# Optimization experiments

Measured on AMD Instinct MI355X. Metric: run time of the kernel, lower is better.

The kernel has to match this reference:

```python
import jax, jax.numpy as jnp
import numpy as np

GROUPS = 32
N_HEADS = 8
EPS = 1e-5


def setup_inputs() -> dict:
    key = jax.random.key(0)
    ks = jax.random.split(key, 4)
    B, C, H, W = 8, 512, 32, 32
    x = jax.random.normal(ks[0], (B, C, H, W), dtype=jnp.float32)
    norm_scale = jnp.ones((C,), jnp.float32)
    norm_bias = jnp.zeros((C,), jnp.float32)
    qkv_w = jax.random.normal(ks[1], (3 * C, C), jnp.float32) * (C ** -0.5)
    qkv_b = jnp.zeros((3 * C,), jnp.float32)
    proj_w = jax.random.normal(ks[2], (C, C), jnp.float32) * (C ** -0.5)
    proj_b = jnp.zeros((C,), jnp.float32)
    return {"x": x, "norm_scale": norm_scale, "norm_bias": norm_bias,
            "qkv_w": qkv_w, "qkv_b": qkv_b, "proj_w": proj_w, "proj_b": proj_b}


def reference(x, norm_scale, norm_bias, qkv_w, qkv_b, proj_w, proj_b):
    B, C, H, W = x.shape
    T = H * W
    xf = x.reshape(B, C, T)

    # GroupNorm32 (32 groups, computed in float32, affine)
    xg = xf.astype(jnp.float32).reshape(B, GROUPS, C // GROUPS, T)
    mean = xg.mean(axis=(2, 3), keepdims=True)
    var = xg.var(axis=(2, 3), keepdims=True)
    xn = ((xg - mean) * jax.lax.rsqrt(var + EPS)).reshape(B, C, T)
    xn = (xn * norm_scale[:, None] + norm_bias[:, None]).astype(x.dtype)

    # qkv: 1x1 conv1d == pointwise matmul -> [B, 3C, T]
    qkv = jnp.einsum('oc,bct->bot', qkv_w, xn) + qkv_b[:, None]

    # QKVAttentionLegacy: reshape to [B*H, 3*ch, T], split
    ch = C // N_HEADS
    qkv_h = qkv.reshape(B * N_HEADS, 3 * ch, T)
    q, k, v = qkv_h[:, :ch], qkv_h[:, ch:2 * ch], qkv_h[:, 2 * ch:]
    scale = ch ** -0.25
    weight = jnp.einsum('bct,bcs->bts', q * scale, k * scale)  # [B*H, T, T]
    weight = jax.nn.softmax(weight.astype(jnp.float32), axis=-1).astype(qkv.dtype)
    a = jnp.einsum('bts,bcs->bct', weight, v).reshape(B, C, T)

    # proj_out (1x1 conv) + residual
    h = jnp.einsum('oc,bct->bot', proj_w, a) + proj_b[:, None]
    return (xf + h).reshape(B, C, H, W)
```

## Files before the change

### kernel.cpp

```cpp
#include <hip/hip_runtime.h>
#include <hip/hip_bf16.h>
#include <stdint.h>

typedef unsigned short u16;
typedef unsigned int u32;
typedef __bf16 bf16x8 __attribute__((ext_vector_type(8)));
typedef float f32x4 __attribute__((ext_vector_type(4)));


static __device__ __forceinline__ u16 f2bf(float f) {
  union { __hip_bfloat16 h; u16 u; } c;
  c.h = __float2bfloat16(f);
  return c.u;
}

static __device__ __forceinline__ void gload_lds16(const void* g, void* l) {
  __builtin_amdgcn_global_load_lds(
      (__attribute__((address_space(1))) u32*)(uintptr_t)g,
      (__attribute__((address_space(3))) u32*)l, 16, 0, 0);
}

__global__ __launch_bounds__(256) void wcvt(const float* __restrict__ wq,
                                            const float* __restrict__ wp,
                                            u16* __restrict__ wqb,
                                            u16* __restrict__ wpb) {
  int idx = (blockIdx.x * 256 + threadIdx.x) * 4;
  const float* s;
  u16* d;
  if (idx < 786432) { s = wq + idx; d = wqb + idx; }
  else { int k = idx - 786432; s = wp + k; d = wpb + k; }
  float4 v = *(const float4*)s;
  uint2 o;
  o.x = (u32)f2bf(v.x) | ((u32)f2bf(v.y) << 16);
  o.y = (u32)f2bf(v.z) | ((u32)f2bf(v.w) << 16);
  *(uint2*)d = o;
}

__global__ __launch_bounds__(256) void gn_stats(const float* __restrict__ x,
                                                float* __restrict__ st) {
  int bg = blockIdx.x;
  const float* p = x + (size_t)bg * 16384;
  float s1 = 0.f, s2 = 0.f;
  for (int i = threadIdx.x * 4; i < 16384; i += 1024) {
    float4 v = *(const float4*)(p + i);
    s1 += v.x + v.y + v.z + v.w;
    s2 += v.x * v.x + v.y * v.y + v.z * v.z + v.w * v.w;
  }
#pragma unroll
  for (int off = 1; off < 64; off <<= 1) {
    s1 += __shfl_xor(s1, off);
    s2 += __shfl_xor(s2, off);
  }
  __shared__ float r1[4], r2[4];
  int w = threadIdx.x >> 6, l = threadIdx.x & 63;
  if (l == 0) { r1[w] = s1; r2[w] = s2; }
  __syncthreads();
  if (threadIdx.x == 0) {
    float t1 = r1[0] + r1[1] + r1[2] + r1[3];
    float t2 = r2[0] + r2[1] + r2[2] + r2[3];
    float mean = t1 * (1.f / 16384.f);
    float var = t2 * (1.f / 16384.f) - mean * mean;
    st[bg * 2] = mean;
    st[bg * 2 + 1] = rsqrtf(var + 1e-5f);
  }
}

__global__ __launch_bounds__(256) void gn_apply(const float* __restrict__ x,
                                                const float* __restrict__ st,
                                                const float* __restrict__ ns,
                                                const float* __restrict__ nbi,
                                                u16* __restrict__ xnt) {
  __shared__ u16 tile[32 * 520];
  int b = blockIdx.x >> 5;
  int t0 = (blockIdx.x & 31) << 5;
  int tid = threadIdx.x;
  int tl = tid & 31, cg = tid >> 5;
#pragma unroll 4
  for (int cc = 0; cc < 64; ++cc) {
    int c = cc * 8 + cg;
    float mean = st[(b * 32 + (c >> 4)) * 2];
    float rstd = st[(b * 32 + (c >> 4)) * 2 + 1];
    float v = x[(size_t)b * 524288 + (size_t)c * 1024 + t0 + tl];
    float vn = (v - mean) * rstd * ns[c] + nbi[c];
    tile[tl * 520 + c] = f2bf(vn);
  }
  __syncthreads();
#pragma unroll
  for (int i = 0; i < 8; ++i) {
    int chunk = i * 256 + tid;
    int tl2 = chunk >> 6;
    int c0 = (chunk & 63) * 8;
    uint4 d = *(const uint4*)(tile + tl2 * 520 + c0);
    *(uint4*)(xnt + (size_t)b * 524288 + (size_t)(t0 + tl2) * 512 + c0) = d;
  }
}

static __device__ __forceinline__ void gemm_core(const u16* Abase, const u16* Bbase,
                                                 f32x4 acc[4][4], u16* As, u16* Bs,
                                                 int w, int l, int wm, int wn) {
  const int r8 = l >> 3, ch = l & 7;
  const int fr = l & 15, fq = l >> 4;
#pragma unroll 1
  for (int kt = 0; kt < 8; ++kt) {
    __syncthreads();
#pragma unroll
    for (int i = 0; i < 4; ++i) {
      int gi = (w << 2) + i;
      int row = (gi << 3) + r8;
      int xoff = ((ch ^ (row & 7)) << 4);
      gload_lds16((const char*)Abase + (size_t)row * 1024 + (kt << 7) + xoff,
                  (char*)As + (gi << 10));
      gload_lds16((const char*)Bbase + (size_t)row * 1024 + (kt << 7) + xoff,
                  (char*)Bs + (gi << 10));
    }
    __syncthreads();
#pragma unroll
    for (int kf = 0; kf < 2; ++kf) {
      bf16x8 af[4], bfv[4];
#pragma unroll
      for (int i = 0; i < 4; ++i) {
        int rowA = wm * 64 + i * 16 + fr;
        af[i] = *(const bf16x8*)(As + rowA * 64 + ((((kf << 2) + fq) ^ (rowA & 7)) << 3));
        int rowB = wn * 64 + i * 16 + fr;
        bfv[i] = *(const bf16x8*)(Bs + rowB * 64 + ((((kf << 2) + fq) ^ (rowB & 7)) << 3));
      }
#pragma unroll
      for (int i = 0; i < 4; ++i)
#pragma unroll
        for (int j = 0; j < 4; ++j)
          acc[i][j] = __builtin_amdgcn_mfma_f32_16x16x32_bf16(af[i], bfv[j], acc[i][j], 0, 0, 0);
    }
  }
}

__global__ __launch_bounds__(256) void gemm_qkv(const u16* __restrict__ Wq,
                                                const u16* __restrict__ Xnt,
                                                const float* __restrict__ bq,
                                                u16* __restrict__ qT,
                                                u16* __restrict__ kT,
                                                u16* __restrict__ vv) {
  __shared__ u16 As[128 * 64];
  __shared__ u16 Bs[128 * 64];
  int bid0 = blockIdx.x;
  int bid = (bid0 & 7) * 96 + (bid0 >> 3);
  int mb = bid % 12, nb = (bid / 12) % 8, b = bid / 96;
  int tid = threadIdx.x, w = tid >> 6, l = tid & 63;
  int wm = w >> 1, wn = w & 1;
  f32x4 acc[4][4];
#pragma unroll
  for (int i = 0; i < 4; ++i)
#pragma unroll
    for (int j = 0; j < 4; ++j) acc[i][j] = (f32x4){0.f, 0.f, 0.f, 0.f};

  gemm_core(Wq + (size_t)mb * 65536, Xnt + (size_t)b * 524288 + (size_t)nb * 65536,
            acc, As, Bs, w, l, wm, wn);

  int fr = l & 15, fq = l >> 4;
#pragma unroll
  for (int i = 0; i < 4; ++i) {
    int o0 = mb * 128 + wm * 64 + i * 16 + fq * 4;
    int h = o0 / 192, j0 = o0 % 192;
    int seg = j0 >> 6, off = j0 & 63;
    float qksc = (seg == 0) ? 0.51011687f : 0.35355339f;
    float b0 = bq[o0], b1 = bq[o0 + 1], b2 = bq[o0 + 2], b3 = bq[o0 + 3];
    size_t hb = (size_t)(b * 8 + h) * 65536;
#pragma unroll
    for (int j = 0; j < 4; ++j) {
      int t = nb * 128 + wn * 64 + j * 16 + fr;
      f32x4 v = acc[i][j];
      if (seg < 2) {
        u16* dst = (seg == 0 ? qT : kT) + hb + (size_t)t * 64 + off;
        uint2 pk;
        pk.x = (u32)f2bf((v[0] + b0) * qksc) | ((u32)f2bf((v[1] + b1) * qksc) << 16);
        pk.y = (u32)f2bf((v[2] + b2) * qksc) | ((u32)f2bf((v[3] + b3) * qksc) << 16);
        *(uint2*)dst = pk;
      } else {
        u16* dst = vv + hb + (size_t)off * 1024 + t;
        dst[0] = f2bf(v[0] + b0);
        dst[1024] = f2bf(v[1] + b1);
        dst[2048] = f2bf(v[2] + b2);
        dst[3072] = f2bf(v[3] + b3);
      }
    }
  }
}

__global__ __launch_bounds__(256) void attn(const u16* __restrict__ qT,
                                            const u16* __restrict__ kT,
                                            const u16* __restrict__ vv,
                                            u16* __restrict__ aT) {
  __shared__ u16 Ks[64 * 64];
  __shared__ u16 Vs[80 * 64];
  __shared__ u16 Ps[4 * 16 * 72];
  int bid = blockIdx.x;
  int bh = (bid & 7) * 8 + (bid >> 7);
  int tq = (bid >> 3) & 15;
  int tid = threadIdx.x, w = tid >> 6, l = tid & 63;
  int fr = l & 15, fq = l >> 4;
  int r8 = l >> 3, ch = l & 7;
  size_t hb = (size_t)bh * 65536;

  {
    int row = 64 + (tid >> 4);
    int c4 = (tid & 15) * 4;
    u16 val = (row == 64) ? (u16)0x3F80 : (u16)0;
    u16* p = Vs + row * 64 + c4;
    p[0] = val; p[1] = val; p[2] = val; p[3] = val;
  }

  bf16x8 aq[2];
  {
    const u16* qp = qT + hb + (size_t)(tq * 64 + w * 16 + fr) * 64 + fq * 8;
    aq[0] = *(const bf16x8*)(qp);
    aq[1] = *(const bf16x8*)(qp + 32);
  }

  f32x4 acc_o[4];
  f32x4 acc_s = (f32x4){0.f, 0.f, 0.f, 0.f};
#pragma unroll
  for (int nb = 0; nb < 4; ++nb) acc_o[nb] = (f32x4){0.f, 0.f, 0.f, 0.f};

  u16* pw = Ps + w * (16 * 72);

  for (int st = 0; st < 16; ++st) {
    __syncthreads();
#pragma unroll
    for (int i = 0; i < 2; ++i) {
      int gi = (w << 1) + i;
      int row = (gi << 3) + r8;
      int xoff = ((ch ^ (row & 7)) << 4);
      gload_lds16((const char*)(kT + hb) + (size_t)(st * 64 + row) * 128 + xoff,
                  (char*)Ks + (gi << 10));
      gload_lds16((const char*)(vv + hb) + (size_t)row * 2048 + st * 128 + xoff,
                  (char*)Vs + (gi << 10));
    }
    __syncthreads();

    f32x4 sa[4];
#pragma unroll
    for (int nb = 0; nb < 4; ++nb) sa[nb] = (f32x4){0.f, 0.f, 0.f, 0.f};
    __builtin_amdgcn_s_setprio(1);
#pragma unroll
    for (int nb = 0; nb < 4; ++nb) {
      int krow = nb * 16 + fr;
#pragma unroll
      for (int kf = 0; kf < 2; ++kf) {
        bf16x8 bk = *(const bf16x8*)(Ks + krow * 64 + ((((kf << 2) + fq) ^ (krow & 7)) << 3));
        sa[nb] = __builtin_amdgcn_mfma_f32_16x16x32_bf16(aq[kf], bk, sa[nb], 0, 0, 0);
      }
    }
    __builtin_amdgcn_s_setprio(0);

#pragma unroll
    for (int nb = 0; nb < 4; ++nb)
#pragma unroll
      for (int r = 0; r < 4; ++r)
        pw[(fq * 4 + r) * 72 + nb * 16 + fr] = f2bf(exp2f(sa[nb][r]));

    bf16x8 ap[2];
#pragma unroll
    for (int kf = 0; kf < 2; ++kf)
      ap[kf] = *(const bf16x8*)(pw + fr * 72 + kf * 32 + fq * 8);

    __builtin_amdgcn_s_setprio(1);
#pragma unroll
    for (int nb = 0; nb < 4; ++nb) {
      int vrow = nb * 16 + fr;
#pragma unroll
      for (int kf = 0; kf < 2; ++kf) {
        bf16x8 bv = *(const bf16x8*)(Vs + vrow * 64 + ((((kf << 2) + fq) ^ (vrow & 7)) << 3));
        acc_o[nb] = __builtin_amdgcn_mfma_f32_16x16x32_bf16(ap[kf], bv, acc_o[nb], 0, 0, 0);
      }
    }
    {
      int vrow = 64 + fr;
#pragma unroll
      for (int kf = 0; kf < 2; ++kf) {
        bf16x8 bv = *(const bf16x8*)(Vs + vrow * 64 + ((((kf << 2) + fq) ^ (vrow & 7)) << 3));
        acc_s = __builtin_amdgcn_mfma_f32_16x16x32_bf16(ap[kf], bv, acc_s, 0, 0, 0);
      }
    }
    __builtin_amdgcn_s_setprio(0);
  }

  int b = bh >> 3, h = bh & 7;
  f32x4 invl;
#pragma unroll
  for (int r = 0; r < 4; ++r) invl[r] = 1.f / __shfl(acc_s[r], l & 48);
#pragma unroll
  for (int nb = 0; nb < 4; ++nb) {
    f32x4 ov = acc_o[nb] * invl;
#pragma unroll
    for (int r = 0; r < 4; ++r) {
      int t = tq * 64 + w * 16 + fq * 4 + r;
      aT[(size_t)b * 524288 + (size_t)t * 512 + h * 64 + nb * 16 + fr] = f2bf(ov[r]);
    }
  }
}

__global__ __launch_bounds__(256) void gemm_proj(const u16* __restrict__ Wp,
                                                 const u16* __restrict__ aT,
                                                 const float* __restrict__ bp,
                                                 const float* __restrict__ x,
                                                 float* __restrict__ out) {
  __shared__ u16 As[128 * 64];
  __shared__ u16 Bs[128 * 64];
  int bid0 = blockIdx.x;
  int bid = (bid0 & 7) * 32 + (bid0 >> 3);
  int mb = bid & 3, nb = (bid >> 2) & 7, b = bid >> 5;
  int tid = threadIdx.x, w = tid >> 6, l = tid & 63;
  int wm = w >> 1, wn = w & 1;
  f32x4 acc[4][4];
#pragma unroll
  for (int i = 0; i < 4; ++i)
#pragma unroll
    for (int j = 0; j < 4; ++j) acc[i][j] = (f32x4){0.f, 0.f, 0.f, 0.f};

  gemm_core(Wp + (size_t)mb * 65536, aT + (size_t)b * 524288 + (size_t)nb * 65536,
            acc, As, Bs, w, l, wm, wn);

  int fr = l & 15, fq = l >> 4;
#pragma unroll
  for (int i = 0; i < 4; ++i) {
    int o0 = mb * 128 + wm * 64 + i * 16 + fq * 4;
    float b0 = bp[o0], b1 = bp[o0 + 1], b2 = bp[o0 + 2], b3 = bp[o0 + 3];
#pragma unroll
    for (int j = 0; j < 4; ++j) {
      int t = nb * 128 + wn * 64 + j * 16 + fr;
      f32x4 v = acc[i][j];
      size_t base = (size_t)b * 524288 + (size_t)o0 * 1024 + t;
      out[base] = x[base] + v[0] + b0;
      out[base + 1024] = x[base + 1024] + v[1] + b1;
      out[base + 2048] = x[base + 2048] + v[2] + b2;
      out[base + 3072] = x[base + 3072] + v[3] + b3;
    }
  }
}

extern "C" void kernel_launch(void* const* d_in, const int* in_sizes, int n_in,
                              void* d_out, int out_size, void* d_ws, size_t ws_size,
                              hipStream_t stream) {
  const float* x = (const float*)d_in[0];
  const float* ns = (const float*)d_in[1];
  const float* nbi = (const float*)d_in[2];
  const float* wq = (const float*)d_in[3];
  const float* bq = (const float*)d_in[4];
  const float* wp = (const float*)d_in[5];
  const float* bp = (const float*)d_in[6];
  float* out = (float*)d_out;
  char* ws = (char*)d_ws;

  u16* wqb = (u16*)(ws);
  u16* wpb = (u16*)(ws + 1572864);
  float* st = (float*)(ws + 2097152);
  u16* xnt = (u16*)(ws + 2101248);
  u16* qT = (u16*)(ws + 2101248 + 8388608);
  u16* kT = (u16*)(ws + 2101248 + 2 * 8388608);
  u16* vv = (u16*)(ws + 2101248 + 3 * 8388608);
  u16* aT = xnt;

  hipLaunchKernelGGL(wcvt, dim3(1024), dim3(256), 0, stream, wq, wp, wqb, wpb);
  hipLaunchKernelGGL(gn_stats, dim3(256), dim3(256), 0, stream, x, st);
  hipLaunchKernelGGL(gn_apply, dim3(256), dim3(256), 0, stream, x, st, ns, nbi, xnt);
  hipLaunchKernelGGL(gemm_qkv, dim3(768), dim3(256), 0, stream, wqb, xnt, bq, qT, kT, vv);
  hipLaunchKernelGGL(attn, dim3(1024), dim3(256), 0, stream, qT, kT, vv, aT);
  hipLaunchKernelGGL(gemm_proj, dim3(256), dim3(256), 0, stream, wpb, aT, bp, x, out);
}
```

Measured before the change: 104.8 us.

## Stage QKV epilogue through LDS and double attention query tile per block

```diff
diff --git a/kernel.cpp b/kernel.cpp
--- a/kernel.cpp
+++ b/kernel.cpp
@@ -139,13 +139,13 @@
                                                 u16* __restrict__ qT,
                                                 u16* __restrict__ kT,
                                                 u16* __restrict__ vv) {
-  __shared__ u16 As[128 * 64];
-  __shared__ u16 Bs[128 * 64];
+  __shared__ u16 SMEM[18432];
   int bid0 = blockIdx.x;
   int bid = (bid0 & 7) * 96 + (bid0 >> 3);
   int mb = bid % 12, nb = (bid / 12) % 8, b = bid / 96;
   int tid = threadIdx.x, w = tid >> 6, l = tid & 63;
-  int wm = w >> 1, wn = w & 1;
+  int wm = tid >> 7, wn = (tid >> 6) & 1;
+  int fr = l & 15, fq = l >> 4;
   f32x4 acc[4][4];
 #pragma unroll
   for (int i = 0; i < 4; ++i)
@@ -153,64 +153,96 @@
     for (int j = 0; j < 4; ++j) acc[i][j] = (f32x4){0.f, 0.f, 0.f, 0.f};
 
   gemm_core(Wq + (size_t)mb * 65536, Xnt + (size_t)b * 524288 + (size_t)nb * 65536,
-            acc, As, Bs, w, l, wm, wn);
-
-  int fr = l & 15, fq = l >> 4;
-#pragma unroll
-  for (int i = 0; i < 4; ++i) {
-    int o0 = mb * 128 + wm * 64 + i * 16 + fq * 4;
-    int h = o0 / 192, j0 = o0 % 192;
-    int seg = j0 >> 6, off = j0 & 63;
-    float qksc = (seg == 0) ? 0.51011687f : 0.35355339f;
-    float b0 = bq[o0], b1 = bq[o0 + 1], b2 = bq[o0 + 2], b3 = bq[o0 + 3];
-    size_t hb = (size_t)(b * 8 + h) * 65536;
-#pragma unroll
-    for (int j = 0; j < 4; ++j) {
-      int t = nb * 128 + wn * 64 + j * 16 + fr;
-      f32x4 v = acc[i][j];
-      if (seg < 2) {
-        u16* dst = (seg == 0 ? qT : kT) + hb + (size_t)t * 64 + off;
-        uint2 pk;
-        pk.x = (u32)f2bf((v[0] + b0) * qksc) | ((u32)f2bf((v[1] + b1) * qksc) << 16);
-        pk.y = (u32)f2bf((v[2] + b2) * qksc) | ((u32)f2bf((v[3] + b3) * qksc) << 16);
-        *(uint2*)dst = pk;
-      } else {
-        u16* dst = vv + hb + (size_t)off * 1024 + t;
-        dst[0] = f2bf(v[0] + b0);
-        dst[1024] = f2bf(v[1] + b1);
-        dst[2048] = f2bf(v[2] + b2);
-        dst[3072] = f2bf(v[3] + b3);
-      }
-    }
-  }
-}
-
-__global__ __launch_bounds__(256) void attn(const u16* __restrict__ qT,
+            acc, SMEM, SMEM + 8192, w, l, wm, wn);
+
+  __syncthreads();
+
+  int seg2 = mb * 2 + wm;
+  int h = seg2 / 3, typ = seg2 % 3;
+  size_t hb = (size_t)(b * 8 + h) * 65536;
+  u16* SUB = SMEM + wm * 9216;
+
+  if (typ < 2) {
+    float qksc = (typ == 0) ? 0.51011687f : 0.35355339f;
+#pragma unroll
+    for (int i = 0; i < 4; ++i) {
+      int oi = i * 16 + fq * 4;
+      float4 bb = *(const float4*)(bq + mb * 128 + wm * 64 + oi);
+#pragma unroll
+      for (int j = 0; j < 4; ++j) {
+        int tl = wn * 64 + j * 16 + fr;
+        f32x4 v = acc[i][j];
+        u32 lo = (u32)f2bf((v[0] + bb.x) * qksc) | ((u32)f2bf((v[1] + bb.y) * qksc) << 16);
+        u32 hi = (u32)f2bf((v[2] + bb.z) * qksc) | ((u32)f2bf((v[3] + bb.w) * qksc) << 16);
+        *(u32*)(SUB + tl * 72 + oi) = lo;
+        *(u32*)(SUB + tl * 72 + oi + 2) = hi;
+      }
+    }
+  } else {
+#pragma unroll
+    for (int i = 0; i < 4; ++i) {
+      int oi = i * 16 + fq * 4;
+      float4 bb = *(const float4*)(bq + mb * 128 + wm * 64 + oi);
+      float bbv[4] = {bb.x, bb.y, bb.z, bb.w};
+#pragma unroll
+      for (int j = 0; j < 4; ++j) {
+        int tl = wn * 64 + j * 16 + fr;
+        f32x4 v = acc[i][j];
+#pragma unroll
+        for (int r = 0; r < 4; ++r)
+          SUB[(oi + r) * 136 + tl] = f2bf(v[r] + bbv[r]);
+      }
+    }
+  }
+  __syncthreads();
+
+  int lt = tid & 127;
+  if (typ < 2) {
+    u16* dstb = (typ == 0 ? qT : kT) + hb;
+#pragma unroll
+    for (int it = 0; it < 8; ++it) {
+      int slot = it * 128 + lt;
+      int t = slot >> 3, chk = slot & 7;
+      uint4 val = *(const uint4*)(SUB + t * 72 + chk * 8);
+      *(uint4*)(dstb + (size_t)(nb * 128 + t) * 64 + chk * 8) = val;
+    }
+  } else {
+#pragma unroll
+    for (int it = 0; it < 8; ++it) {
+      int slot = it * 128 + lt;
+      int c = slot >> 4, chk = slot & 15;
+      uint4 val = *(const uint4*)(SUB + c * 136 + chk * 8);
+      *(uint4*)(vv + hb + (size_t)c * 1024 + nb * 128 + chk * 8) = val;
+    }
+  }
+}
+
+__global__ __launch_bounds__(512) void attn(const u16* __restrict__ qT,
                                             const u16* __restrict__ kT,
                                             const u16* __restrict__ vv,
                                             u16* __restrict__ aT) {
   __shared__ u16 Ks[64 * 64];
   __shared__ u16 Vs[80 * 64];
-  __shared__ u16 Ps[4 * 16 * 72];
+  __shared__ u16 Ps[8 * 16 * 72];
   int bid = blockIdx.x;
-  int bh = (bid & 7) * 8 + (bid >> 7);
-  int tq = (bid >> 3) & 15;
+  int bh = (bid & 7) * 8 + (bid >> 6);
+  int tq = (bid >> 3) & 7;
   int tid = threadIdx.x, w = tid >> 6, l = tid & 63;
   int fr = l & 15, fq = l >> 4;
   int r8 = l >> 3, ch = l & 7;
   size_t hb = (size_t)bh * 65536;
 
   {
-    int row = 64 + (tid >> 4);
-    int c4 = (tid & 15) * 4;
+    int row = 64 + (tid >> 5);
+    int c2 = (tid & 31) * 2;
     u16 val = (row == 64) ? (u16)0x3F80 : (u16)0;
-    u16* p = Vs + row * 64 + c4;
-    p[0] = val; p[1] = val; p[2] = val; p[3] = val;
+    Vs[row * 64 + c2] = val;
+    Vs[row * 64 + c2 + 1] = val;
   }
 
   bf16x8 aq[2];
   {
-    const u16* qp = qT + hb + (size_t)(tq * 64 + w * 16 + fr) * 64 + fq * 8;
+    const u16* qp = qT + hb + (size_t)(tq * 128 + w * 16 + fr) * 64 + fq * 8;
     aq[0] = *(const bf16x8*)(qp);
     aq[1] = *(const bf16x8*)(qp + 32);
   }
@@ -224,15 +256,13 @@
 
   for (int st = 0; st < 16; ++st) {
     __syncthreads();
-#pragma unroll
-    for (int i = 0; i < 2; ++i) {
-      int gi = (w << 1) + i;
-      int row = (gi << 3) + r8;
+    {
+      int row = (w << 3) + r8;
       int xoff = ((ch ^ (row & 7)) << 4);
       gload_lds16((const char*)(kT + hb) + (size_t)(st * 64 + row) * 128 + xoff,
-                  (char*)Ks + (gi << 10));
+                  (char*)Ks + (w << 10));
       gload_lds16((const char*)(vv + hb) + (size_t)row * 2048 + st * 128 + xoff,
-                  (char*)Vs + (gi << 10));
+                  (char*)Vs + (w << 10));
     }
     __syncthreads();
 
@@ -292,7 +322,7 @@
     f32x4 ov = acc_o[nb] * invl;
 #pragma unroll
     for (int r = 0; r < 4; ++r) {
-      int t = tq * 64 + w * 16 + fq * 4 + r;
+      int t = tq * 128 + w * 16 + fq * 4 + r;
       aT[(size_t)b * 524288 + (size_t)t * 512 + h * 64 + nb * 16 + fr] = f2bf(ov[r]);
     }
   }
@@ -363,6 +393,6 @@
   hipLaunchKernelGGL(gn_stats, dim3(256), dim3(256), 0, stream, x, st);
   hipLaunchKernelGGL(gn_apply, dim3(256), dim3(256), 0, stream, x, st, ns, nbi, xnt);
   hipLaunchKernelGGL(gemm_qkv, dim3(768), dim3(256), 0, stream, wqb, xnt, bq, qT, kT, vv);
-  hipLaunchKernelGGL(attn, dim3(1024), dim3(256), 0, stream, qT, kT, vv, aT);
+  hipLaunchKernelGGL(attn, dim3(512), dim3(512), 0, stream, qT, kT, vv, aT);
   hipLaunchKernelGGL(gemm_proj, dim3(256), dim3(256), 0, stream, wpb, aT, bp, x, out);
 }
```

Result: faster. 95.96 us (-8.5%).
